# Performance work log

Measured on AMD Instinct MI355X. Metric: run time of the kernel, lower is better.

Reference implementation:

```python
import jax, jax.numpy as jnp
import numpy as np

LEAKY_SLOPE = 0.2  # DGL GATConv default negative_slope


def setup_inputs() -> dict:
    key = jax.random.key(0)
    ks = jax.random.split(key, 10)
    N_SRC, N_DST, E = 100000, 100000, 1600000
    H1, H0, D = 2, 2, 32          # in_h1_heads, in_h0_heads (GAT num_heads), out_dim
    IN1, IN0 = 128, 128           # in_h1_dim, in_h0_dim
    OUT_HEADS = 4
    return {
        "hier_1": jax.random.normal(ks[0], (N_SRC, H1, IN1), jnp.float32),
        "hier_0": jax.random.normal(ks[1], (N_DST, IN0), jnp.float32),
        "src_idx": jax.random.randint(ks[2], (E,), 0, N_SRC, jnp.int32),
        "dst_idx": jax.random.randint(ks[3], (E,), 0, N_DST, jnp.int32),
        "W_src": jax.random.normal(ks[4], (H0 * D, IN1), jnp.float32) * 0.05,
        "W_dst": jax.random.normal(ks[5], (H0 * D, IN0), jnp.float32) * 0.05,
        "attn_l": jax.random.normal(ks[6], (H0, D), jnp.float32) * 0.1,
        "attn_r": jax.random.normal(ks[7], (H0, D), jnp.float32) * 0.1,
        "gat_bias": jnp.zeros((H0, D), jnp.float32),
        "fc_W": jax.random.normal(ks[8], (OUT_HEADS, H1 * H0), jnp.float32),
        "fc_b": jnp.zeros((OUT_HEADS,), jnp.float32),
    }


def reference(hier_1, hier_0, src_idx, dst_idx, W_src, W_dst,
              attn_l, attn_r, gat_bias, fc_W, fc_b):
    N_src, H1, _ = hier_1.shape
    N_dst = hier_0.shape[0]
    H0, D = attn_l.shape

    # Shared GATConv projections (same weights reused across the H1 python loop
    # in the original -> vectorize over the H1 axis).
    feat_src = jnp.einsum('nhi,oi->nho', hier_1, W_src).reshape(N_src, H1, H0, D)
    feat_dst = (hier_0 @ W_dst.T).reshape(N_dst, H0, D)

    el = jnp.einsum('nhkd,kd->nhk', feat_src, attn_l)   # [N_src, H1, H0]
    er = jnp.einsum('nkd,kd->nk', feat_dst, attn_r)     # [N_dst, H0]

    # Edge attention logits + softmax over incoming edges per dst node.
    e = jax.nn.leaky_relu(el[src_idx] + er[dst_idx][:, None, :], LEAKY_SLOPE)  # [E,H1,H0]
    emax = jax.ops.segment_max(e, dst_idx, num_segments=N_dst)
    emax = jnp.where(jnp.isfinite(emax), emax, 0.0)     # zero-in-degree safety
    ee = jnp.exp(e - emax[dst_idx])
    denom = jax.ops.segment_sum(ee, dst_idx, num_segments=N_dst)
    alpha = ee / denom[dst_idx]                          # [E, H1, H0]

    # Aggregate messages: sum_e alpha * feat_src[src].
    msg = alpha[..., None] * feat_src[src_idx]           # [E, H1, H0, D]
    out = jax.ops.segment_sum(msg, dst_idx, num_segments=N_dst)  # [N_dst,H1,H0,D]
    out = out + gat_bias[None, None]                     # GATConv bias (per call)

    # cat over H1 (H1-major), transpose, softmax-normalized linear head mixing.
    res = out.reshape(N_dst, H1 * H0, D)
    res = jnp.swapaxes(res, 1, 2)                        # [N_dst, D, H1*H0]
    W = jax.nn.softmax(fc_W, axis=1)                     # normWeight: softmax(dim=1)
    res = res @ W.T + fc_b                               # [N_dst, D, out_heads]
    return jnp.swapaxes(res, 1, 2)                       # [N_dst, out_heads, D]
```

## Files before the change

### kernel.cpp

```cpp
#include <hip/hip_runtime.h>
#include <hip/hip_bf16.h>

__device__ __forceinline__ float lrelu(float x) { return x > 0.f ? x : 0.2f * x; }
__device__ __forceinline__ float blo(unsigned u) { return __uint_as_float(u << 16); }
__device__ __forceinline__ float bhi(unsigned u) { return __uint_as_float(u & 0xffff0000u); }

__global__ void k_prep(const float* __restrict__ Wdst,
                       const float* __restrict__ attn_r,
                       const float* __restrict__ fcW,
                       const float* __restrict__ fcb,
                       float* __restrict__ w_er, float* __restrict__ Wn,
                       float* __restrict__ fb) {
    int t = threadIdx.x;
    if (t < 256) {
        int h0 = t >> 7, i = t & 127;
        float s = 0.f;
        for (int d = 0; d < 32; ++d)
            s += attn_r[h0 * 32 + d] * Wdst[(size_t)(h0 * 32 + d) * 128 + i];
        w_er[t] = s;
    }
    if (t < 16) {
        int oh = t >> 2, k = t & 3;
        float w[4], m = -1e30f;
        for (int j = 0; j < 4; ++j) {
            w[j] = fcW[oh * 4 + j];
            m = fmaxf(m, w[j]);
        }
        float s = 0.f;
        for (int j = 0; j < 4; ++j) s += __expf(w[j] - m);
        Wn[t] = __expf(w[k] - m) / s;
    }
    if (t < 4) fb[t] = fcb[t];
}

__global__ __launch_bounds__(256) void k_featA(
        const float* __restrict__ hier1, const float* __restrict__ Wsrc,
        const float* __restrict__ attn_l,
        const float* __restrict__ hier0, const float* __restrict__ w_er,
        const int* __restrict__ dstIdx,
        __hip_bfloat16* __restrict__ featb, float* __restrict__ el,
        float* __restrict__ er, int* __restrict__ deg,
        int nrows, int Ndst, int E) {
    __shared__ float4 Wlds[2048];
    __shared__ float4 Hlds[1024];
    int t = threadIdx.x;

    {
        int e = blockIdx.x * 256 + t;
        if (e < E) atomicAdd(&deg[dstIdx[e]], 1);
    }

    const float4* W4 = reinterpret_cast<const float4*>(Wsrc);
#pragma unroll
    for (int j = 0; j < 8; ++j) {
        int g = t + j * 256;
        Wlds[(g & 31) * 64 + (g >> 5)] = W4[g];
    }
    int base = blockIdx.x * 32;
    const float4* H4 = reinterpret_cast<const float4*>(hier1);
#pragma unroll
    for (int j = 0; j < 4; ++j) {
        int idx = t + j * 256;
        int r = idx >> 5;
        if (base + r < nrows)
            Hlds[idx] = H4[(size_t)(base + r) * 32 + (idx & 31)];
    }
    __syncthreads();

    int w = t >> 6, o = t & 63;
    float al = attn_l[o];
    float acc[8];
#pragma unroll
    for (int j = 0; j < 8; ++j) acc[j] = 0.f;

    for (int kk = 0; kk < 32; ++kk) {
        float4 wv = Wlds[kk * 64 + o];
#pragma unroll
        for (int j = 0; j < 8; ++j) {
            float4 hv = Hlds[(w * 8 + j) * 32 + kk];
            acc[j] = fmaf(hv.x, wv.x,
                     fmaf(hv.y, wv.y,
                     fmaf(hv.z, wv.z,
                     fmaf(hv.w, wv.w, acc[j]))));
        }
    }

#pragma unroll
    for (int j = 0; j < 8; ++j) {
        int row = base + w * 8 + j;
        if (row < nrows) {
            featb[((size_t)(row >> 1)) * 128 + (row & 1) * 64 + o] =
                __float2bfloat16(acc[j]);
            float v = acc[j] * al;
#pragma unroll
            for (int m = 16; m >= 1; m >>= 1) v += __shfl_xor(v, m, 64);
            if ((o & 31) == 0) el[row * 2 + (o >> 5)] = v;
        }
    }

    int lane = t & 63;
    int gw = blockIdx.x * 4 + w;
    int nwaves = gridDim.x * 4;
    float2 w0 = *reinterpret_cast<const float2*>(w_er + lane * 2);
    float2 w1 = *reinterpret_cast<const float2*>(w_er + 128 + lane * 2);
    for (int node = gw; node < Ndst; node += nwaves) {
        float2 h = *reinterpret_cast<const float2*>(hier0 + (size_t)node * 128 + lane * 2);
        float p0 = h.x * w0.x + h.y * w0.y;
        float p1 = h.x * w1.x + h.y * w1.y;
#pragma unroll
        for (int m = 32; m >= 1; m >>= 1) {
            p0 += __shfl_xor(p0, m, 64);
            p1 += __shfl_xor(p1, m, 64);
        }
        if (lane == 0) {
            er[node * 2] = p0;
            er[node * 2 + 1] = p1;
        }
    }
}

__global__ void k_alloc(const int* __restrict__ deg, int* __restrict__ off,
                        int* __restrict__ cursor, int* __restrict__ counter,
                        int N) {
    int d = blockIdx.x * blockDim.x + threadIdx.x;
    int lane = threadIdx.x & 63;
    int v = (d < N) ? deg[d] : 0;
    int inc = v;
#pragma unroll
    for (int m = 1; m < 64; m <<= 1) {
        int u = __shfl_up(inc, m, 64);
        if (lane >= m) inc += u;
    }
    int excl = inc - v;
    int base = 0;
    if (lane == 63) base = atomicAdd(counter, inc);
    base = __shfl(base, 63, 64);
    if (d < N) {
        off[d] = base + excl;
        cursor[d] = base + excl;
    }
}

__global__ void k_scatter(const int* __restrict__ src, const int* __restrict__ dst,
                          int* __restrict__ cursor, int* __restrict__ ssrc, int E) {
    int e = blockIdx.x * blockDim.x + threadIdx.x;
    if (e >= E) return;
    int pos = atomicAdd(&cursor[dst[e]], 1);
    ssrc[pos] = src[e];
}

__global__ __launch_bounds__(256) void k_gather(
        const int* __restrict__ ssrc, const int* __restrict__ off,
        const int* __restrict__ deg,
        const float* __restrict__ el, const float* __restrict__ er,
        const uint4* __restrict__ feat4,
        const float* __restrict__ bias,
        const float* __restrict__ Wn, const float* __restrict__ fb,
        float* __restrict__ out, int Ndst, int E) {
    __shared__ float g[4][128];
    int t = threadIdx.x;
    int wv = t >> 6, lane = t & 63;
    int d = blockIdx.x * 4 + wv;
    bool valid = d < Ndst;

    int q = lane >> 4;
    int c = lane & 15;
    int k = c >> 2;
    float erk = valid ? er[d * 2 + (k & 1)] : 0.f;
    int start = valid ? off[d] : 0;
    int n = valid ? deg[d] : 0;

    float a[8];
#pragma unroll
    for (int j = 0; j < 8; ++j) a[j] = 0.f;
    float den = 0.f;

    int ai = start + q;
    int s_pre = ssrc[ai < E ? ai : 0];
    for (int i = 0; i < n; i += 4) {
        int s = s_pre;
        int ni = start + i + 4 + q;
        s_pre = ssrc[ni < E ? ni : 0];
        bool ve = (i + q) < n;
        uint4 f = feat4[(size_t)s * 16 + c];
        float eL = el[s * 4 + k];
        float ee = ve ? __expf(lrelu(eL + erk)) : 0.f;
        den += ee;
        a[0] = fmaf(ee, blo(f.x), a[0]);
        a[1] = fmaf(ee, bhi(f.x), a[1]);
        a[2] = fmaf(ee, blo(f.y), a[2]);
        a[3] = fmaf(ee, bhi(f.y), a[3]);
        a[4] = fmaf(ee, blo(f.z), a[4]);
        a[5] = fmaf(ee, bhi(f.z), a[5]);
        a[6] = fmaf(ee, blo(f.w), a[6]);
        a[7] = fmaf(ee, bhi(f.w), a[7]);
    }

#pragma unroll
    for (int m = 16; m <= 32; m <<= 1) {
        den += __shfl_xor(den, m, 64);
#pragma unroll
        for (int j = 0; j < 8; ++j) a[j] += __shfl_xor(a[j], m, 64);
    }

    float inv = den > 0.f ? 1.f / den : 0.f;
    if (q == 0) {
        int h0 = k & 1, ddb = (c & 3) * 8;
#pragma unroll
        for (int j = 0; j < 8; ++j)
            g[wv][c * 8 + j] = a[j] * inv + bias[h0 * 32 + ddb + j];
    }
    __syncthreads();

    if (valid) {
        int dd = (lane & 15) * 2;
        int oh = lane >> 4;
        float r0 = fb[oh], r1 = r0;
#pragma unroll
        for (int kk = 0; kk < 4; ++kk) {
            float wgt = Wn[oh * 4 + kk];
            r0 = fmaf(g[wv][kk * 32 + dd], wgt, r0);
            r1 = fmaf(g[wv][kk * 32 + dd + 1], wgt, r1);
        }
        *reinterpret_cast<float2*>(out + (size_t)d * 128 + lane * 2) =
            make_float2(r0, r1);
    }
}

extern "C" void kernel_launch(void* const* d_in, const int* in_sizes, int n_in,
                              void* d_out, int out_size, void* d_ws, size_t ws_size,
                              hipStream_t stream) {
    (void)n_in; (void)out_size; (void)ws_size;
    const float* hier1  = (const float*)d_in[0];
    const float* hier0  = (const float*)d_in[1];
    const int*   srcIdx = (const int*)d_in[2];
    const int*   dstIdx = (const int*)d_in[3];
    const float* Wsrc   = (const float*)d_in[4];
    const float* Wdst   = (const float*)d_in[5];
    const float* attn_l = (const float*)d_in[6];
    const float* attn_r = (const float*)d_in[7];
    const float* bias   = (const float*)d_in[8];
    const float* fcW    = (const float*)d_in[9];
    const float* fcb    = (const float*)d_in[10];
    float* out = (float*)d_out;

    const int Nsrc  = in_sizes[0] / 256;
    const int Ndst  = in_sizes[1] / 128;
    const int E     = in_sizes[2];
    const int nrows = Nsrc * 2;

    __hip_bfloat16* featb = (__hip_bfloat16*)d_ws;
    float* el   = (float*)(featb + (size_t)Nsrc * 128);
    float* er   = el   + (size_t)nrows * 2;
    float* w_er = er   + (size_t)Ndst * 2;
    float* Wn   = w_er + 256;
    float* fb   = Wn + 16;
    int*  deg     = (int*)(fb + 4);
    int*  off     = deg + Ndst;
    int*  cursor  = off + Ndst;
    int*  counter = cursor + Ndst;
    int*  ssrc    = counter + 1;

    hipMemsetAsync(deg, 0, (size_t)Ndst * sizeof(int), stream);
    hipMemsetAsync(counter, 0, sizeof(int), stream);

    k_prep<<<1, 256, 0, stream>>>(Wdst, attn_r, fcW, fcb, w_er, Wn, fb);

    int blocksA = (nrows + 31) / 32;
    int blocksE = (E + 255) / 256;
    if (blocksE > blocksA) blocksA = blocksE;
    k_featA<<<blocksA, 256, 0, stream>>>(hier1, Wsrc, attn_l, hier0, w_er,
                                         dstIdx, featb, el, er, deg,
                                         nrows, Ndst, E);

    k_alloc<<<(Ndst + 255) / 256, 256, 0, stream>>>(deg, off, cursor, counter, Ndst);

    k_scatter<<<(E + 255) / 256, 256, 0, stream>>>(srcIdx, dstIdx, cursor, ssrc, E);

    k_gather<<<(Ndst + 3) / 4, 256, 0, stream>>>(ssrc, off, deg, el, er,
                                                 (const uint4*)featb,
                                                 bias, Wn, fb, out, Ndst, E);
}
```

Baseline: 564.0 us.

## Use split-bf16 MFMA for source feature projection instead of FP32 FMAs

The src projection GEMM in k_featA moves from LDS-tiled scalar FP32 FMAs to 16x16x32 bf16 MFMA instructions. Each FP32 value is split into bf16 hi and lo parts, and three MFMAs (hi*hi, hi*lo, lo*hi) per chunk keep accuracy near FP32. W_src is pre-split into bf16 hi/lo buffers in k_prep. The grid is resized to one wave per 16-row tile, with grid-stride loops for the degree atomics and the er computation. This cuts ALU cost of the projection, but the launch now has fewer blocks and B operands are read straight from global memory with no LDS reuse.

```diff
diff --git a/kernel.cpp b/kernel.cpp
--- a/kernel.cpp
+++ b/kernel.cpp
@@ -1,18 +1,39 @@
 #include <hip/hip_runtime.h>
 #include <hip/hip_bf16.h>
+
+typedef __attribute__((ext_vector_type(8))) short short8_t;
+typedef __attribute__((ext_vector_type(4))) float float4v;
 
 __device__ __forceinline__ float lrelu(float x) { return x > 0.f ? x : 0.2f * x; }
 __device__ __forceinline__ float blo(unsigned u) { return __uint_as_float(u << 16); }
 __device__ __forceinline__ float bhi(unsigned u) { return __uint_as_float(u & 0xffff0000u); }
+
+__device__ __forceinline__ short8_t mk8(unsigned a, unsigned b, unsigned c, unsigned d) {
+    union { unsigned u[4]; short8_t s; } x;
+    x.u[0] = a; x.u[1] = b; x.u[2] = c; x.u[3] = d;
+    return x.s;
+}
 
 __global__ void k_prep(const float* __restrict__ Wdst,
                        const float* __restrict__ attn_r,
                        const float* __restrict__ fcW,
                        const float* __restrict__ fcb,
+                       const float* __restrict__ Wsrc,
                        float* __restrict__ w_er, float* __restrict__ Wn,
-                       float* __restrict__ fb) {
+                       float* __restrict__ fb,
+                       unsigned short* __restrict__ Wb_hi,
+                       unsigned short* __restrict__ Wb_lo) {
     int t = threadIdx.x;
-    if (t < 256) {
+#pragma unroll
+    for (int j = 0; j < 32; ++j) {
+        int i = t + j * 256;
+        float x = Wsrc[i];
+        unsigned hb = __float_as_uint(x) & 0xffff0000u;
+        float lf = x - __uint_as_float(hb);
+        Wb_hi[i] = (unsigned short)(hb >> 16);
+        Wb_lo[i] = (unsigned short)(__float_as_uint(lf) >> 16);
+    }
+    {
         int h0 = t >> 7, i = t & 127;
         float s = 0.f;
         for (int d = 0; d < 32; ++d)
@@ -34,71 +55,101 @@
 }
 
 __global__ __launch_bounds__(256) void k_featA(
-        const float* __restrict__ hier1, const float* __restrict__ Wsrc,
+        const float* __restrict__ hier1,
+        const unsigned short* __restrict__ Wb_hi,
+        const unsigned short* __restrict__ Wb_lo,
         const float* __restrict__ attn_l,
         const float* __restrict__ hier0, const float* __restrict__ w_er,
         const int* __restrict__ dstIdx,
         __hip_bfloat16* __restrict__ featb, float* __restrict__ el,
         float* __restrict__ er, int* __restrict__ deg,
-        int nrows, int Ndst, int E) {
-    __shared__ float4 Wlds[2048];
-    __shared__ float4 Hlds[1024];
+        int nrows, int Ndst, int E, int ntiles) {
     int t = threadIdx.x;
-
-    {
-        int e = blockIdx.x * 256 + t;
-        if (e < E) atomicAdd(&deg[dstIdx[e]], 1);
-    }
-
-    const float4* W4 = reinterpret_cast<const float4*>(Wsrc);
-#pragma unroll
-    for (int j = 0; j < 8; ++j) {
-        int g = t + j * 256;
-        Wlds[(g & 31) * 64 + (g >> 5)] = W4[g];
-    }
-    int base = blockIdx.x * 32;
-    const float4* H4 = reinterpret_cast<const float4*>(hier1);
-#pragma unroll
-    for (int j = 0; j < 4; ++j) {
-        int idx = t + j * 256;
-        int r = idx >> 5;
-        if (base + r < nrows)
-            Hlds[idx] = H4[(size_t)(base + r) * 32 + (idx & 31)];
-    }
-    __syncthreads();
-
-    int w = t >> 6, o = t & 63;
-    float al = attn_l[o];
-    float acc[8];
-#pragma unroll
-    for (int j = 0; j < 8; ++j) acc[j] = 0.f;
-
-    for (int kk = 0; kk < 32; ++kk) {
-        float4 wv = Wlds[kk * 64 + o];
-#pragma unroll
-        for (int j = 0; j < 8; ++j) {
-            float4 hv = Hlds[(w * 8 + j) * 32 + kk];
-            acc[j] = fmaf(hv.x, wv.x,
-                     fmaf(hv.y, wv.y,
-                     fmaf(hv.z, wv.z,
-                     fmaf(hv.w, wv.w, acc[j]))));
-        }
-    }
-
-#pragma unroll
-    for (int j = 0; j < 8; ++j) {
-        int row = base + w * 8 + j;
-        if (row < nrows) {
-            featb[((size_t)(row >> 1)) * 128 + (row & 1) * 64 + o] =
-                __float2bfloat16(acc[j]);
-            float v = acc[j] * al;
-#pragma unroll
-            for (int m = 16; m >= 1; m >>= 1) v += __shfl_xor(v, m, 64);
-            if ((o & 31) == 0) el[row * 2 + (o >> 5)] = v;
-        }
-    }
-
-    int lane = t & 63;
+    int w = t >> 6, lane = t & 63;
+
+    for (int e = blockIdx.x * 256 + t; e < E; e += gridDim.x * 256)
+        atomicAdd(&deg[dstIdx[e]], 1);
+
+    int lr = lane & 15;
+    int lg = lane >> 4;
+
+    for (int tile = blockIdx.x * 4 + w; tile < ntiles; tile += gridDim.x * 4) {
+        int m0 = tile * 16;
+
+        short8_t a_hi[4], a_lo[4];
+        int row_l = m0 + lr;
+        if (row_l >= nrows) row_l = nrows - 1;
+        const float* hrow = hier1 + (size_t)row_l * 128 + lg * 8;
+#pragma unroll
+        for (int kc = 0; kc < 4; ++kc) {
+            float4 f0 = *reinterpret_cast<const float4*>(hrow + kc * 32);
+            float4 f1 = *reinterpret_cast<const float4*>(hrow + kc * 32 + 4);
+            float xs[8] = {f0.x, f0.y, f0.z, f0.w, f1.x, f1.y, f1.z, f1.w};
+            unsigned h[4], l4[4];
+#pragma unroll
+            for (int p = 0; p < 4; ++p) {
+                unsigned b0 = __float_as_uint(xs[2 * p]);
+                unsigned b1 = __float_as_uint(xs[2 * p + 1]);
+                unsigned h0b = b0 & 0xffff0000u, h1b = b1 & 0xffff0000u;
+                h[p] = (h0b >> 16) | h1b;
+                float l0 = xs[2 * p] - __uint_as_float(h0b);
+                float l1 = xs[2 * p + 1] - __uint_as_float(h1b);
+                l4[p] = (__float_as_uint(l0) >> 16) | (__float_as_uint(l1) & 0xffff0000u);
+            }
+            a_hi[kc] = mk8(h[0], h[1], h[2], h[3]);
+            a_lo[kc] = mk8(l4[0], l4[1], l4[2], l4[3]);
+        }
+
+        float4v acc[4];
+#pragma unroll
+        for (int n = 0; n < 4; ++n) acc[n] = (float4v){0.f, 0.f, 0.f, 0.f};
+#pragma unroll
+        for (int n = 0; n < 4; ++n) {
+            const unsigned short* bh = Wb_hi + (size_t)(n * 16 + lr) * 128 + lg * 8;
+            const unsigned short* bl = Wb_lo + (size_t)(n * 16 + lr) * 128 + lg * 8;
+#pragma unroll
+            for (int kc = 0; kc < 4; ++kc) {
+                short8_t Bh = *reinterpret_cast<const short8_t*>(bh + kc * 32);
+                short8_t Bl = *reinterpret_cast<const short8_t*>(bl + kc * 32);
+                acc[n] = __builtin_amdgcn_mfma_f32_16x16x32_bf16(a_lo[kc], Bh, acc[n], 0, 0, 0);
+                acc[n] = __builtin_amdgcn_mfma_f32_16x16x32_bf16(a_hi[kc], Bl, acc[n], 0, 0, 0);
+                acc[n] = __builtin_amdgcn_mfma_f32_16x16x32_bf16(a_hi[kc], Bh, acc[n], 0, 0, 0);
+            }
+        }
+
+        float pe0[4] = {0.f, 0.f, 0.f, 0.f};
+        float pe1[4] = {0.f, 0.f, 0.f, 0.f};
+#pragma unroll
+        for (int n = 0; n < 4; ++n) {
+            float al = attn_l[n * 16 + lr];
+#pragma unroll
+            for (int r = 0; r < 4; ++r) {
+                int row = m0 + lg * 4 + r;
+                float v = acc[n][r];
+                if (row < nrows)
+                    featb[((size_t)(row >> 1)) * 128 + (row & 1) * 64 + n * 16 + lr] =
+                        __float2bfloat16(v);
+                if (n < 2) pe0[r] += v * al; else pe1[r] += v * al;
+            }
+        }
+#pragma unroll
+        for (int m = 1; m <= 8; m <<= 1) {
+#pragma unroll
+            for (int r = 0; r < 4; ++r) {
+                pe0[r] += __shfl_xor(pe0[r], m, 64);
+                pe1[r] += __shfl_xor(pe1[r], m, 64);
+            }
+        }
+        if (lr < 2) {
+#pragma unroll
+            for (int r = 0; r < 4; ++r) {
+                int row = m0 + lg * 4 + r;
+                float ev = lr ? pe1[r] : pe0[r];
+                if (row < nrows) el[row * 2 + lr] = ev;
+            }
+        }
+    }
+
     int gw = blockIdx.x * 4 + w;
     int nwaves = gridDim.x * 4;
     float2 w0 = *reinterpret_cast<const float2*>(w_er + lane * 2);
@@ -248,9 +299,12 @@
     const int Ndst  = in_sizes[1] / 128;
     const int E     = in_sizes[2];
     const int nrows = Nsrc * 2;
+    const int ntiles = (nrows + 15) / 16;
 
     __hip_bfloat16* featb = (__hip_bfloat16*)d_ws;
-    float* el   = (float*)(featb + (size_t)Nsrc * 128);
+    unsigned short* Wb_hi = (unsigned short*)(featb + (size_t)Nsrc * 128);
+    unsigned short* Wb_lo = Wb_hi + 8192;
+    float* el   = (float*)(Wb_lo + 8192);
     float* er   = el   + (size_t)nrows * 2;
     float* w_er = er   + (size_t)Ndst * 2;
     float* Wn   = w_er + 256;
@@ -264,14 +318,15 @@
     hipMemsetAsync(deg, 0, (size_t)Ndst * sizeof(int), stream);
     hipMemsetAsync(counter, 0, sizeof(int), stream);
 
-    k_prep<<<1, 256, 0, stream>>>(Wdst, attn_r, fcW, fcb, w_er, Wn, fb);
-
-    int blocksA = (nrows + 31) / 32;
-    int blocksE = (E + 255) / 256;
-    if (blocksE > blocksA) blocksA = blocksE;
-    k_featA<<<blocksA, 256, 0, stream>>>(hier1, Wsrc, attn_l, hier0, w_er,
-                                         dstIdx, featb, el, er, deg,
-                                         nrows, Ndst, E);
+    k_prep<<<1, 256, 0, stream>>>(Wdst, attn_r, fcW, fcb, Wsrc,
+                                  w_er, Wn, fb, Wb_hi, Wb_lo);
+
+    int blocksA = (ntiles + 3) / 4;
+    if (blocksA < 1) blocksA = 1;
+    k_featA<<<blocksA, 256, 0, stream>>>(hier1, Wb_hi, Wb_lo, attn_l,
+                                         hier0, w_er, dstIdx,
+                                         featb, el, er, deg,
+                                         nrows, Ndst, E, ntiles);
 
     k_alloc<<<(Ndst + 255) / 256, 256, 0, stream>>>(deg, off, cursor, counter, Ndst);
 
```

Result: faster. 523.6 us (-7.2%).
